# Performance work log

Measured on AMD Instinct MI355X. Metric: run time of the kernel, lower is better.

Reference implementation:

```python
import jax, jax.numpy as jnp
import numpy as np

N_TOKENS = 32768
D_MODEL = 1024
NUM_CODES = 4096
CODE_DEPTH = 256


def setup_inputs() -> dict:
    key = jax.random.key(0)
    kx, kc, kw, kb = jax.random.split(key, 4)
    x = jax.random.normal(kx, (N_TOKENS, D_MODEL), dtype=jnp.float32)
    # codebook init mirrors the torch module: randn, row-normalized, first column zeroed
    cb = jax.random.normal(kc, (NUM_CODES, CODE_DEPTH), dtype=jnp.float32)
    cb = cb / jnp.linalg.norm(cb, axis=-1, keepdims=True)
    cb = cb.at[:, 0].set(0.0)
    W_down = jax.random.normal(kw, (D_MODEL, CODE_DEPTH), dtype=jnp.float32) * (D_MODEL ** -0.5)
    b_down = jax.random.normal(kb, (CODE_DEPTH,), dtype=jnp.float32) * 0.01
    return {"x": x, "codebook": cb, "W_down": W_down, "b_down": b_down}


def reference(x, codebook, W_down, b_down):
    # downsample d_model -> code_depth, then L2-normalize (eps=1e-6)
    z = x @ W_down + b_down                                   # [N, D]
    z = z / (jnp.linalg.norm(z, axis=-1, keepdims=True) + 1e-6)
    # squared euclidean distances to codebook[1:] (argmin of sq == argmin of cdist)
    cb = codebook[1:]                                         # [K-1, D]
    sq = (jnp.sum(z * z, axis=-1, keepdims=True)
          - 2.0 * (z @ cb.T)
          + jnp.sum(cb * cb, axis=-1))                        # [N, K-1]
    code_indices = jnp.argmin(sq, axis=-1) + 1                # [N], in [1, K)
    hard_codes = codebook[code_indices]                       # [N, D] gather
    return z, code_indices, hard_codes
```

## Files before the change

### kernel.cpp

```cpp
#include <hip/hip_runtime.h>
#include <math.h>
#include <stdint.h>

#define NT 32768
#define DM 1024
#define NC 4096
#define CD 256

#define X_F4 (DM/4)
#define W_F4 (CD/4)
#define Z_F4 (CD/4)
#define C_F4 (CD/4)

#define TILE_B 17408

typedef __attribute__((ext_vector_type(8))) short bf16x8;
typedef __attribute__((ext_vector_type(4))) float floatx4;
typedef __attribute__((ext_vector_type(16))) float floatx16;

__device__ __forceinline__ unsigned short f2bf(float f) {
    union { float f; uint32_t u; } v; v.f = f;
    uint32_t u = v.u;
    u += 0x7FFFu + ((u >> 16) & 1u);
    return (unsigned short)(u >> 16);
}

__device__ __forceinline__ void split8(const float4 f0, const float4 f1,
                                       bf16x8& h, bf16x8& l) {
    float f[8] = {f0.x, f0.y, f0.z, f0.w, f1.x, f1.y, f1.z, f1.w};
    #pragma unroll
    for (int j = 0; j < 8; ++j) {
        union { float f; uint32_t u; } v; v.f = f[j];
        h[j] = (short)(v.u >> 16);
        union { uint32_t u; float f; } t; t.u = v.u & 0xFFFF0000u;
        l[j] = (short)f2bf(f[j] - t.f);
    }
}

__global__ __launch_bounds__(256) void k0_prep(const float4* __restrict__ cb,
                                               ushort* __restrict__ cbb2) {
    int tid = threadIdx.x;
    int l = tid & 63, wid = tid >> 6;
    int code = blockIdx.x * 8 + wid * 2 + (l >> 5);
    int fr = l & 31, f = fr >> 1, hi = fr & 1;
    const float4* p = cb + (size_t)code * C_F4 + f * 4 + hi * 2;
    float4 f0 = p[0], f1 = p[1];
    bf16x8 h;
    h[0] = (short)f2bf(f0.x); h[1] = (short)f2bf(f0.y);
    h[2] = (short)f2bf(f0.z); h[3] = (short)f2bf(f0.w);
    h[4] = (short)f2bf(f1.x); h[5] = (short)f2bf(f1.y);
    h[6] = (short)f2bf(f1.z); h[7] = (short)f2bf(f1.w);
    float ss = f0.x*f0.x + f0.y*f0.y + f0.z*f0.z + f0.w*f0.w
             + f1.x*f1.x + f1.y*f1.y + f1.z*f1.z + f1.w*f1.w;
    #pragma unroll
    for (int m = 16; m >= 1; m >>= 1) ss += __shfl_xor(ss, m, 64);
    int ct = code >> 5, r = code & 31;
    char* base = (char*)cbb2 + (size_t)ct * TILE_B;
    *(bf16x8*)(base + f * 1024 + (((hi << 5) | r) << 4)) = h;
    if (fr == 0) {
        float nh = 2.0f - 0.5f * ss;
        union { float f; uint32_t u; } v; v.f = nh;
        uint32_t uh = v.u & 0xFFFF0000u;
        union { uint32_t u; float f; } t; t.u = uh;
        bf16x8 e = (bf16x8){0, 0, 0, 0, 0, 0, 0, 0};
        e[0] = (short)(uh >> 16);
        e[1] = (short)f2bf(nh - t.f);
        *(bf16x8*)(base + 16 * 1024 + (r << 4)) = e;
    } else if (fr == 1) {
        bf16x8 z = (bf16x8){0, 0, 0, 0, 0, 0, 0, 0};
        *(bf16x8*)(base + 16 * 1024 + ((32 | r) << 4)) = z;
    }
}

__global__ __launch_bounds__(256) void k0b_wsplit(const float4* __restrict__ W,
                                                  ushort* __restrict__ WTh,
                                                  ushort* __restrict__ WTl) {
    __shared__ float lds[16][260];
    int slab = blockIdx.x;
    int tid = threadIdx.x;
    #pragma unroll
    for (int jj = 0; jj < 4; ++jj) {
        int v = jj * 256 + tid;
        int row = v >> 6, f4 = v & 63;
        float4 d = W[(size_t)(slab * 16 + row) * W_F4 + f4];
        *(float4*)&lds[row][f4 * 4] = d;
    }
    __syncthreads();
    int c = tid;
    #pragma unroll
    for (int kb = 0; kb < 2; ++kb) {
        bf16x8 h, l;
        #pragma unroll
        for (int j = 0; j < 8; ++j) {
            float x = lds[kb * 8 + j][c];
            union { float f; uint32_t u; } v; v.f = x;
            h[j] = (short)(v.u >> 16);
            union { uint32_t u; float f; } t; t.u = v.u & 0xFFFF0000u;
            l[j] = (short)f2bf(x - t.f);
        }
        size_t off = (size_t)c * 1024 + slab * 16 + kb * 8;
        *(bf16x8*)(WTh + off) = h;
        *(bf16x8*)(WTl + off) = l;
    }
}

__global__ __launch_bounds__(256, 2) void k1_gemm1(const float4* __restrict__ X,
                                                   const ushort* __restrict__ WTh,
                                                   const ushort* __restrict__ WTl,
                                                   float4* __restrict__ Zp) {
    __shared__ __align__(16) char lds[65536];
    char* Ah = lds;
    char* Al = lds + 16384;
    char* Bh = lds + 32768;
    char* Bl = lds + 49152;

    int tid  = threadIdx.x;
    int w    = tid >> 6, lane = tid & 63;
    int wm   = w >> 1, wn = w & 1;
    int c    = lane & 15, q = lane >> 4;
    int mb   = blockIdx.x >> 1, nb = blockIdx.x & 1;
    int m0   = mb * 128;
    int n0   = nb * 128;

    auto issue_loads = [&](int kt, float4* ga, bf16x8* gbh, bf16x8* gbl) {
        #pragma unroll
        for (int jj = 0; jj < 4; ++jj) {
            int v = jj * 256 + tid;
            int row = v >> 3, ch = v & 7;
            const float4* p = X + (size_t)(m0 + row) * X_F4 + kt * 16 + ch * 2;
            ga[jj * 2]     = p[0];
            ga[jj * 2 + 1] = p[1];
        }
        #pragma unroll
        for (int jj = 0; jj < 4; ++jj) {
            int v = jj * 256 + tid;
            int col = v >> 3, ch = v & 7;
            size_t off = (size_t)(n0 + col) * 1024 + kt * 64 + ch * 8;
            gbh[jj] = *(const bf16x8*)(WTh + off);
            gbl[jj] = *(const bf16x8*)(WTl + off);
        }
    };
    auto write_lds = [&](const float4* ga, const bf16x8* gbh, const bf16x8* gbl) {
        #pragma unroll
        for (int jj = 0; jj < 4; ++jj) {
            int v = jj * 256 + tid;
            int row = v >> 3, ch = v & 7;
            bf16x8 h, l;
            split8(ga[jj * 2], ga[jj * 2 + 1], h, l);
            int off = row * 128 + ((ch ^ (row & 7)) << 4);
            *(bf16x8*)(Ah + off) = h;
            *(bf16x8*)(Al + off) = l;
        }
        #pragma unroll
        for (int jj = 0; jj < 4; ++jj) {
            int v = jj * 256 + tid;
            int col = v >> 3, ch = v & 7;
            int off = col * 128 + ((ch ^ (col & 7)) << 4);
            *(bf16x8*)(Bh + off) = gbh[jj];
            *(bf16x8*)(Bl + off) = gbl[jj];
        }
    };

    floatx4 acc[4][4];
    #pragma unroll
    for (int i = 0; i < 4; ++i)
        #pragma unroll
        for (int j = 0; j < 4; ++j) acc[i][j] = (floatx4){0.f, 0.f, 0.f, 0.f};

    float4 ga[8]; bf16x8 gbh[4], gbl[4];
    issue_loads(0, ga, gbh, gbl);
    write_lds(ga, gbh, gbl);

    for (int kt = 0; kt < 16; ++kt) {
        __syncthreads();
        if (kt < 15) issue_loads(kt + 1, ga, gbh, gbl);

        #pragma unroll
        for (int ks = 0; ks < 2; ++ks) {
            bf16x8 xh[4], xl[4], wh[4], wl[4];
            #pragma unroll
            for (int i = 0; i < 4; ++i) {
                int xrow = wm * 64 + i * 16 + c;
                int xoff = xrow * 128 + (((ks * 4 + q) ^ (xrow & 7)) << 4);
                xh[i] = *(const bf16x8*)(Ah + xoff);
                xl[i] = *(const bf16x8*)(Al + xoff);
                int wrow = wn * 64 + i * 16 + c;
                int woff = wrow * 128 + (((ks * 4 + q) ^ (wrow & 7)) << 4);
                wh[i] = *(const bf16x8*)(Bh + woff);
                wl[i] = *(const bf16x8*)(Bl + woff);
            }
            #pragma unroll
            for (int xi = 0; xi < 4; ++xi)
                #pragma unroll
                for (int ni = 0; ni < 4; ++ni) {
                    acc[xi][ni] = __builtin_amdgcn_mfma_f32_16x16x32_bf16(wh[ni], xh[xi], acc[xi][ni], 0, 0, 0);
                    acc[xi][ni] = __builtin_amdgcn_mfma_f32_16x16x32_bf16(wh[ni], xl[xi], acc[xi][ni], 0, 0, 0);
                    acc[xi][ni] = __builtin_amdgcn_mfma_f32_16x16x32_bf16(wl[ni], xh[xi], acc[xi][ni], 0, 0, 0);
                }
        }

        __syncthreads();
        if (kt < 15) write_lds(ga, gbh, gbl);
    }

    #pragma unroll
    for (int xi = 0; xi < 4; ++xi) {
        int tok = m0 + wm * 64 + xi * 16 + c;
        #pragma unroll
        for (int ni = 0; ni < 4; ++ni) {
            int nf4 = nb * 32 + wn * 16 + ni * 4 + q;
            float4 o;
            o.x = acc[xi][ni][0]; o.y = acc[xi][ni][1];
            o.z = acc[xi][ni][2]; o.w = acc[xi][ni][3];
            Zp[(size_t)tok * Z_F4 + nf4] = o;
        }
    }
}

__global__ __launch_bounds__(256) void k1b_norm(float4* __restrict__ Z,
                                                const float4* __restrict__ bias) {
    int wid = threadIdx.x >> 6, lane = threadIdx.x & 63;
    int t = blockIdx.x * 4 + wid;
    float4 b = bias[lane];
    float4 z = Z[(size_t)t * Z_F4 + lane];
    z.x += b.x; z.y += b.y; z.z += b.z; z.w += b.w;
    double ss = (double)z.x*z.x + (double)z.y*z.y + (double)z.z*z.z + (double)z.w*z.w;
    #pragma unroll
    for (int m = 32; m >= 1; m >>= 1) ss += __shfl_xor(ss, m, 64);
    float inv = 1.0f / ((float)sqrt(ss) + 1e-6f);
    z.x *= inv; z.y *= inv; z.z *= inv; z.w *= inv;
    Z[(size_t)t * Z_F4 + lane] = z;
}

__global__ __launch_bounds__(256, 2) void k2_mfma(const float* __restrict__ Z,
                                                  const ushort* __restrict__ Cbb2,
                                                  int4* __restrict__ cands) {
    __shared__ uint32_t Mk[64][4][4];

    int tid  = threadIdx.x;
    int w    = tid >> 6;
    int wm   = w >> 1;
    int wc   = w & 1;
    int lane = tid & 63;
    int r    = lane & 31;
    int hi   = lane >> 5;
    int t0   = blockIdx.x * 64;

    bf16x8 Bt[17];
    #pragma unroll
    for (int f = 0; f < 16; ++f) {
        const float* zp = Z + (size_t)(t0 + wm * 32 + r) * CD + f * 16 + hi * 8;
        float4 f0 = *(const float4*)zp;
        float4 f1 = *(const float4*)(zp + 4);
        bf16x8 b;
        b[0] = (short)f2bf(f0.x); b[1] = (short)f2bf(f0.y);
        b[2] = (short)f2bf(f0.z); b[3] = (short)f2bf(f0.w);
        b[4] = (short)f2bf(f1.x); b[5] = (short)f2bf(f1.y);
        b[6] = (short)f2bf(f1.z); b[7] = (short)f2bf(f1.w);
        Bt[f] = b;
    }
    {
        bf16x8 b = (bf16x8){0, 0, 0, 0, 0, 0, 0, 0};
        if (hi == 0) { b[0] = (short)0x3F80; b[1] = (short)0x3F80; }
        Bt[16] = b;
    }

    const char* half = (const char*)Cbb2 + (size_t)(wc * 64) * TILE_B;
    int l0 = (wc == 0 && r == 0) ? (lane + 1) : lane;
    const char* ap0 = half + l0 * 16;
    const char* apL = half + lane * 16;

    float K1f = 0.0f, K2f = 0.0f, K3f = 0.0f, K4f = 0.0f;

    bf16x8 A0[17], A1[17];
    #pragma unroll
    for (int f = 0; f < 17; ++f) A0[f] = *(const bf16x8*)(ap0 + f * 1024);

    const char* ap = apL + TILE_B;

    auto compute = [&](const bf16x8 (&Ax)[17], int ct) {
        floatx16 Cc;
        #pragma unroll
        for (int i = 0; i < 16; ++i) Cc[i] = 0.0f;
        #pragma unroll
        for (int f = 0; f < 17; ++f)
            Cc = __builtin_amdgcn_mfma_f32_32x32x16_bf16(Ax[f], Bt[f], Cc, 0, 0, 0);
        #pragma unroll
        for (int reg = 0; reg < 16; ++reg) {
            union { float f; uint32_t u; } uv; uv.f = Cc[reg];
            uint32_t ku = (uv.u & 0xFFFFF800u) | ((uint32_t)ct << 4) | (uint32_t)reg;
            union { uint32_t u; float f; } kv; kv.u = ku;
            float k = kv.f;
            K4f = __builtin_amdgcn_fmed3f(K3f, K4f, k);
            K3f = __builtin_amdgcn_fmed3f(K2f, K3f, k);
            K2f = __builtin_amdgcn_fmed3f(K1f, K2f, k);
            K1f = fmaxf(K1f, k);
        }
    };

    for (int ctl = 0; ctl < 64; ctl += 2) {
        #pragma unroll
        for (int f = 0; f < 17; ++f) A1[f] = *(const bf16x8*)(ap + f * 1024);
        ap += TILE_B;
        compute(A0, wc * 64 + ctl);
        const char* apn = (ctl + 2 < 64) ? ap : apL;
        #pragma unroll
        for (int f = 0; f < 17; ++f) A0[f] = *(const bf16x8*)(apn + f * 1024);
        ap += TILE_B;
        compute(A1, wc * 64 + ctl + 1);
        if ((ctl & 15) == 14) __builtin_amdgcn_s_barrier();
    }

    {
        int lt = wm * 32 + r, src = wc * 2 + hi;
        union { float f; uint32_t u; } a, b, c, d;
        a.f = K1f; b.f = K2f; c.f = K3f; d.f = K4f;
        Mk[lt][src][0] = a.u; Mk[lt][src][1] = b.u;
        Mk[lt][src][2] = c.u; Mk[lt][src][3] = d.u;
    }
    __syncthreads();

    if (tid < 64) {
        uint32_t bk0 = 0, bk1 = 0, bk2 = 0, bk3 = 0;
        uint32_t be0 = 0, be1 = 0, be2 = 0, be3 = 0;
        #pragma unroll
        for (int s = 0; s < 4; ++s) {
            #pragma unroll
            for (int j = 0; j < 4; ++j) {
                uint32_t key = Mk[tid][s][j];
                uint32_t e = (uint32_t)s;
                if (key > bk0) {
                    bk3 = bk2; be3 = be2; bk2 = bk1; be2 = be1;
                    bk1 = bk0; be1 = be0; bk0 = key; be0 = e;
                } else if (key > bk1) {
                    bk3 = bk2; be3 = be2; bk2 = bk1; be2 = be1; bk1 = key; be1 = e;
                } else if (key > bk2) {
                    bk3 = bk2; be3 = be2; bk2 = key; be2 = e;
                } else if (key > bk3) {
                    bk3 = key; be3 = e;
                }
            }
        }
        auto dec = [&](uint32_t key, uint32_t e) -> int {
            int ct = (int)((key >> 4) & 127u);
            int rg = (int)(key & 15u);
            int row = (rg & 3) + 8 * (rg >> 2) + 4 * (int)(e & 1);
            int code = ct * 32 + row;
            return code < 1 ? 1 : code;
        };
        int4 out;
        out.x = dec(bk0, be0); out.y = dec(bk1, be1);
        out.z = dec(bk2, be2); out.w = dec(bk3, be3);
        cands[t0 + tid] = out;
    }
}

__global__ __launch_bounds__(256) void k3_refine(const float4* __restrict__ Z,
                                                 const float4* __restrict__ Cb,
                                                 const int4* __restrict__ cands,
                                                 float* __restrict__ idxOut,
                                                 float4* __restrict__ hardOut) {
    int wid = threadIdx.x >> 6, lane = threadIdx.x & 63;
    int t = blockIdx.x * 4 + wid;
    int4 cd = cands[t];
    int cc[4] = {cd.x, cd.y, cd.z, cd.w};
    float4 z = Z[(size_t)t * Z_F4 + lane];
    double best = -1.0e300;
    int bi = NC;
    #pragma unroll
    for (int e = 0; e < 4; ++e) {
        int idx = cc[e];
        float4 cf = Cb[(size_t)idx * C_F4 + lane];
        double dot = (double)z.x*cf.x + (double)z.y*cf.y + (double)z.z*cf.z + (double)z.w*cf.w;
        double nrm = (double)cf.x*cf.x + (double)cf.y*cf.y + (double)cf.z*cf.z + (double)cf.w*cf.w;
        #pragma unroll
        for (int m = 32; m >= 1; m >>= 1) {
            dot += __shfl_xor(dot, m, 64);
            nrm += __shfl_xor(nrm, m, 64);
        }
        double s = dot - 0.5 * nrm;
        if (idx >= 1 && (s > best || (s == best && idx < bi))) { best = s; bi = idx; }
    }
    if (lane == 0) idxOut[t] = (float)bi;
    hardOut[(size_t)t * C_F4 + lane] = Cb[(size_t)bi * C_F4 + lane];
}

extern "C" void kernel_launch(void* const* d_in, const int* in_sizes, int n_in,
                              void* d_out, int out_size, void* d_ws, size_t ws_size,
                              hipStream_t stream) {
    const float* x  = (const float*)d_in[0];
    const float* cb = (const float*)d_in[1];
    const float* w  = (const float*)d_in[2];
    const float* bd = (const float*)d_in[3];

    float* zOut    = (float*)d_out;
    float* idxOut  = zOut + (size_t)NT * CD;
    float* hardOut = idxOut + NT;

    int4*   cands = (int4*)d_ws;
    ushort* cbb2  = (ushort*)((char*)d_ws + 524288);
    ushort* wth   = (ushort*)((char*)d_ws + 2752512);
    ushort* wtl   = (ushort*)((char*)d_ws + 3276800);

    k0_prep<<<NC / 8, 256, 0, stream>>>((const float4*)cb, cbb2);
    k0b_wsplit<<<DM / 16, 256, 0, stream>>>((const float4*)w, wth, wtl);
    k1_gemm1<<<(NT / 128) * 2, 256, 0, stream>>>((const float4*)x, wth, wtl,
                                                 (float4*)zOut);
    k1b_norm<<<NT / 4, 256, 0, stream>>>((float4*)zOut, (const float4*)bd);
    k2_mfma<<<NT / 64, 256, 0, stream>>>(zOut, cbb2, cands);
    k3_refine<<<NT / 4, 256, 0, stream>>>((const float4*)zOut, (const float4*)cb,
                                          cands, idxOut, (float4*)hardOut);
}
```

Measured before the change: 392.2 us.

## Stage codebook tiles into LDS via direct global-to-LDS loads with double buffering

Instead of each wave loading all 17 codebook fragments into registers (duplicated across the two row-waves sharing a column half), the block now cooperatively stages each tile into a double-buffered LDS region using global_load_lds. The two waves that share a tile each fetch half of it. Manual vmcnt waits and barriers guard each buffer. This halves global/L2 traffic for the codebook and frees registers, at the cost of LDS reads, two barriers per tile, and about 70 KB of shared memory, which may limit occupancy below the requested two blocks per CU.

```diff
diff --git a/kernel.cpp b/kernel.cpp
--- a/kernel.cpp
+++ b/kernel.cpp
@@ -23,6 +23,12 @@
     uint32_t u = v.u;
     u += 0x7FFFu + ((u >> 16) & 1u);
     return (unsigned short)(u >> 16);
+}
+
+__device__ __forceinline__ void gload_lds16(const void* g, void* l) {
+    __builtin_amdgcn_global_load_lds(
+        (const __attribute__((address_space(1))) void*)g,
+        (__attribute__((address_space(3))) void*)l, 16, 0, 0);
 }
 
 __device__ __forceinline__ void split8(const float4 f0, const float4 f1,
@@ -235,6 +241,7 @@
 __global__ __launch_bounds__(256, 2) void k2_mfma(const float* __restrict__ Z,
                                                   const ushort* __restrict__ Cbb2,
                                                   int4* __restrict__ cands) {
+    __shared__ __align__(16) char sbuf[69632];
     __shared__ uint32_t Mk[64][4][4];
 
     int tid  = threadIdx.x;
@@ -265,26 +272,34 @@
         Bt[16] = b;
     }
 
-    const char* half = (const char*)Cbb2 + (size_t)(wc * 64) * TILE_B;
-    int l0 = (wc == 0 && r == 0) ? (lane + 1) : lane;
-    const char* ap0 = half + l0 * 16;
-    const char* apL = half + lane * 16;
+    char* myStream = sbuf + wc * 34816;
+
+    auto stage = [&](int gt, char* dst) {
+        const char* tb = (const char*)Cbb2 + (size_t)gt * TILE_B;
+        int lo = lane * 16;
+        if (gt == 0 && (lane & 31) == 0) lo += 16;
+        if (wm == 0) {
+            #pragma unroll
+            for (int f = 0; f < 9; ++f)
+                gload_lds16(tb + f * 1024 + lo, dst + f * 1024);
+        } else {
+            #pragma unroll
+            for (int f = 9; f < 17; ++f)
+                gload_lds16(tb + f * 1024 + lo, dst + f * 1024);
+        }
+    };
 
     float K1f = 0.0f, K2f = 0.0f, K3f = 0.0f, K4f = 0.0f;
 
-    bf16x8 A0[17], A1[17];
-    #pragma unroll
-    for (int f = 0; f < 17; ++f) A0[f] = *(const bf16x8*)(ap0 + f * 1024);
-
-    const char* ap = apL + TILE_B;
-
-    auto compute = [&](const bf16x8 (&Ax)[17], int ct) {
+    auto computeT = [&](const char* sb, int ct) {
         floatx16 Cc;
         #pragma unroll
         for (int i = 0; i < 16; ++i) Cc[i] = 0.0f;
         #pragma unroll
-        for (int f = 0; f < 17; ++f)
-            Cc = __builtin_amdgcn_mfma_f32_32x32x16_bf16(Ax[f], Bt[f], Cc, 0, 0, 0);
+        for (int f = 0; f < 17; ++f) {
+            bf16x8 Af = *(const bf16x8*)(sb + f * 1024 + lane * 16);
+            Cc = __builtin_amdgcn_mfma_f32_32x32x16_bf16(Af, Bt[f], Cc, 0, 0, 0);
+        }
         #pragma unroll
         for (int reg = 0; reg < 16; ++reg) {
             union { float f; uint32_t u; } uv; uv.f = Cc[reg];
@@ -298,17 +313,18 @@
         }
     };
 
-    for (int ctl = 0; ctl < 64; ctl += 2) {
-        #pragma unroll
-        for (int f = 0; f < 17; ++f) A1[f] = *(const bf16x8*)(ap + f * 1024);
-        ap += TILE_B;
-        compute(A0, wc * 64 + ctl);
-        const char* apn = (ctl + 2 < 64) ? ap : apL;
-        #pragma unroll
-        for (int f = 0; f < 17; ++f) A0[f] = *(const bf16x8*)(apn + f * 1024);
-        ap += TILE_B;
-        compute(A1, wc * 64 + ctl + 1);
-        if ((ctl & 15) == 14) __builtin_amdgcn_s_barrier();
+    stage(wc * 64 + 0, myStream);
+    stage(wc * 64 + 1, myStream + 17408);
+
+    for (int ctl = 0; ctl < 64; ++ctl) {
+        if (wm == 0) { asm volatile("s_waitcnt vmcnt(9)" ::: "memory"); }
+        else         { asm volatile("s_waitcnt vmcnt(8)" ::: "memory"); }
+        __builtin_amdgcn_s_barrier();
+
+        computeT(myStream + (ctl & 1) * 17408, wc * 64 + ctl);
+
+        __builtin_amdgcn_s_barrier();
+        stage(wc * 64 + ((ctl + 2) & 63), myStream + (ctl & 1) * 17408);
     }
 
     {
```

Measured after the change: 398.5 us. No clear change (+1.6%).
